# Kernel optimization log

Hardware: AMD Instinct MI355X
Metric: run time of the kernel (lower is better)

Reference implementation:

```python
import jax, jax.numpy as jnp
import numpy as np

N = 4096      # num_nodes (also node feature dim)
E = 32768     # num_edges
EMB = 8       # embedding_dim


def setup_inputs() -> dict:
    key = jax.random.key(0)
    ks = jax.random.split(key, 12)
    s = lambda fan_in: 1.0 / np.sqrt(fan_in)
    return {
        "x": jax.random.normal(ks[0], (N, N), dtype=jnp.float32),
        "edge_index": jax.random.randint(ks[1], (2, E), 0, N, dtype=jnp.int64),
        "edge_weight": jax.random.uniform(ks[2], (E,), dtype=jnp.float32),
        # GCNConv linear (PyG Linear, weight [out,in]) + bias
        "gcn_w": jax.random.normal(ks[3], (N, N), dtype=jnp.float32) * s(N),
        "gcn_b": jnp.zeros((N,), dtype=jnp.float32),
        # Wq: Linear(N -> E)
        "wq_w": jax.random.normal(ks[4], (E, N), dtype=jnp.float32) * s(N),
        "wq_b": jax.random.normal(ks[5], (E,), dtype=jnp.float32) * s(N),
        # edge embedding table [E, EMB]
        "emb": jax.random.normal(ks[6], (E, EMB), dtype=jnp.float32),
        # WF: Linear(N+EMB -> 1)
        "wf_w": jax.random.normal(ks[7], (1, N + EMB), dtype=jnp.float32) * s(N + EMB),
        "wf_b": jax.random.normal(ks[8], (1,), dtype=jnp.float32) * s(N + EMB),
    }


def reference(x, edge_index, edge_weight, gcn_w, gcn_b, wq_w, wq_b, emb, wf_w, wf_b):
    n = x.shape[0]
    row, col = edge_index[0], edge_index[1]
    # --- GCNConv: add self loops (weight 1.0), symmetric normalization ---
    loop = jnp.arange(n)
    row_f = jnp.concatenate([row, loop])
    col_f = jnp.concatenate([col, loop])
    w_f = jnp.concatenate([edge_weight, jnp.ones((n,), dtype=x.dtype)])
    deg = jax.ops.segment_sum(w_f, col_f, num_segments=n)          # weighted in-degree
    dis = jnp.where(deg > 0, jax.lax.rsqrt(deg), 0.0)              # deg^{-1/2}, 0 for isolated
    norm = dis[row_f] * w_f * dis[col_f]                           # [E+N]
    h = x @ gcn_w.T                                                # linear transform first (as PyG)
    agg = jax.ops.segment_sum(norm[:, None] * h[row_f], col_f, num_segments=n)
    H1 = jnp.tanh(agg + gcn_b)                                     # [N, N]
    # --- dense head ---
    H2 = jnp.tanh(H1 @ wq_w.T + wq_b)                              # [N, E]
    H2_t = H2.T                                                    # [E, N]
    feat = jnp.concatenate([H2_t, emb], axis=1)                    # [E, N+EMB]
    F_hat = (feat @ wf_w.T + wf_b)[:, 0]                           # [E]
    return F_hat
```

## Files before the change

kernel.cpp:

```cpp
#include <hip/hip_runtime.h>
#include <hip/hip_bf16.h>

#define NN 4096
#define NE 32768
#define NEMB 8

typedef __bf16 bf16x8 __attribute__((ext_vector_type(8)));
typedef float  f32x4  __attribute__((ext_vector_type(4)));

__device__ __forceinline__ unsigned short f2bf(float f) {
  union { float f; unsigned int u; } v; v.f = f;
  return (unsigned short)((v.u + 0x7FFFu + ((v.u >> 16) & 1u)) >> 16);
}

__global__ void k_f2bf(const float* __restrict__ in, unsigned short* __restrict__ out, long n8) {
  long i = (long)blockIdx.x * blockDim.x + threadIdx.x;
  long stride = (long)gridDim.x * blockDim.x;
  for (long j = i; j < n8; j += stride) {
    const float* p = in + j * 8;
    float4 a = *(const float4*)p;
    float4 b = *(const float4*)(p + 4);
    union { unsigned short u[8]; uint4 v; } o;
    o.u[0] = f2bf(a.x); o.u[1] = f2bf(a.y); o.u[2] = f2bf(a.z); o.u[3] = f2bf(a.w);
    o.u[4] = f2bf(b.x); o.u[5] = f2bf(b.y); o.u[6] = f2bf(b.z); o.u[7] = f2bf(b.w);
    *(uint4*)(out + j * 8) = o.v;
  }
}

__global__ void k_deg_init(float* deg) { deg[blockIdx.x * 256 + threadIdx.x] = 1.0f; }

__global__ void k_edge_accum(const int* __restrict__ ei, const float* __restrict__ ew,
                             float* deg, int* cnt) {
  int e = blockIdx.x * 256 + threadIdx.x;
  if (e >= NE) return;
  int c = ei[NE + e];
  atomicAdd(&deg[c], ew[e]);
  atomicAdd(&cnt[c], 1);
}

__global__ void k_dis(const float* __restrict__ deg, float* __restrict__ dis) {
  int i = blockIdx.x * 256 + threadIdx.x;
  float d = deg[i];
  dis[i] = d > 0.f ? rsqrtf(d) : 0.f;
}

__global__ void k_scan(const int* __restrict__ cnt, int* __restrict__ starts) {
  __shared__ int sh[1024];
  int tid = threadIdx.x;
  int base = tid * 4;
  int v[4]; int sum = 0;
  for (int i = 0; i < 4; i++) { v[i] = cnt[base + i]; sum += v[i]; }
  sh[tid] = sum;
  __syncthreads();
  for (int offd = 1; offd < 1024; offd <<= 1) {
    int t = (tid >= offd) ? sh[tid - offd] : 0;
    __syncthreads();
    sh[tid] += t;
    __syncthreads();
  }
  int run = sh[tid] - sum;
  for (int i = 0; i < 4; i++) { starts[base + i] = run; run += v[i]; }
}

__global__ void k_fill(const int* __restrict__ ei, const int* __restrict__ starts,
                       int* cursor, int* csr_e) {
  int e = blockIdx.x * 256 + threadIdx.x;
  if (e >= NE) return;
  int c = ei[NE + e];
  int pos = atomicAdd(&cursor[c], 1);
  csr_e[starts[c] + pos] = e;
}

__global__ void k_sortnorm(const int* __restrict__ ei, const float* __restrict__ ew,
                           const int* __restrict__ starts, const int* __restrict__ cnt,
                           const float* __restrict__ dis,
                           int* csr_e, int* __restrict__ csr_row, float* __restrict__ csr_nrm) {
  int n = blockIdx.x * 256 + threadIdx.x;
  if (n >= NN) return;
  int s = starts[n], c = cnt[n];
  for (int i = 1; i < c; i++) {
    int key = csr_e[s + i]; int j = i - 1;
    while (j >= 0 && csr_e[s + j] > key) { csr_e[s + j + 1] = csr_e[s + j]; j--; }
    csr_e[s + j + 1] = key;
  }
  float dn = dis[n];
  for (int i = 0; i < c; i++) {
    int e = csr_e[s + i];
    int r = ei[e];
    csr_row[s + i] = r;
    csr_nrm[s + i] = dis[r] * ew[e] * dn;
  }
}

__global__ __launch_bounds__(256) void k_agg(
    const float* __restrict__ h, const float* __restrict__ dis,
    const int* __restrict__ starts, const int* __restrict__ cnt,
    const int* __restrict__ csr_row, const float* __restrict__ csr_nrm,
    const float* __restrict__ gcn_b, unsigned short* __restrict__ H1b) {
  int n = blockIdx.x;
  int tid = threadIdx.x;
  float dn = dis[n];
  float sw = dn * dn;
  float acc[16];
  const float* hn = h + (size_t)n * NN;
  #pragma unroll
  for (int i = 0; i < 16; i++) { int f = tid + i * 256; acc[i] = sw * hn[f] + gcn_b[f]; }
  int s = starts[n], c = cnt[n];
  __shared__ int   s_row[64];
  __shared__ float s_nrm[64];
  for (int base = 0; base < c; base += 64) {
    int m = min(64, c - base);
    __syncthreads();
    if (tid < m) { s_row[tid] = csr_row[s + base + tid]; s_nrm[tid] = csr_nrm[s + base + tid]; }
    __syncthreads();
    for (int j = 0; j < m; j++) {
      const float* hr = h + (size_t)s_row[j] * NN;
      float wgt = s_nrm[j];
      #pragma unroll
      for (int i = 0; i < 16; i++) acc[i] += wgt * hr[tid + i * 256];
    }
  }
  #pragma unroll
  for (int i = 0; i < 16; i++)
    H1b[(size_t)n * NN + tid + i * 256] = f2bf(tanhf(acc[i]));
}

__device__ __forceinline__ void gload16(const void* g, void* l) {
  __builtin_amdgcn_global_load_lds(
      (const __attribute__((address_space(1))) unsigned int*)g,
      (__attribute__((address_space(3))) unsigned int*)l, 16, 0, 0);
}

#define BARX() do { __builtin_amdgcn_sched_barrier(0); __builtin_amdgcn_s_barrier(); __builtin_amdgcn_sched_barrier(0); } while (0)
#define LGKM0() do { asm volatile("s_waitcnt lgkmcnt(0)" ::: "memory"); __builtin_amdgcn_sched_barrier(0); } while (0)
#define VMC(n) do { asm volatile("s_waitcnt vmcnt(" #n ")" ::: "memory"); } while (0)


#define STAGE(buf, mat, kk, tk) do { \
    size_t off_ = (size_t)(tk) * 64 + (kk) * 32; \
    gload16((mat ? gB0 : gA0) + off_, &LDS[buf][mat][kk][c0][0]); \
    gload16((mat ? gB1 : gA1) + off_, &LDS[buf][mat][kk][c0 + 1][0]); \
  } while (0)

#define LDA4(dst, buf, kk, q) do { \
    const unsigned short* b_ = &LDS[buf][0][kk][wr * 8 + (q) * 4][0] + aoff; \
    dst[0] = *(const bf16x8*)(b_); \
    dst[1] = *(const bf16x8*)(b_ + 512); \
    dst[2] = *(const bf16x8*)(b_ + 1024); \
    dst[3] = *(const bf16x8*)(b_ + 1536); \
  } while (0)

#define LDB4(dst, buf, kk) do { \
    const unsigned short* b_ = &LDS[buf][1][kk][wc * 4][0] + aoff; \
    dst[0] = *(const bf16x8*)(b_); \
    dst[1] = *(const bf16x8*)(b_ + 512); \
    dst[2] = *(const bf16x8*)(b_ + 1024); \
    dst[3] = *(const bf16x8*)(b_ + 1536); \
  } while (0)

#define MMA16(q, av, bv) do { \
    __builtin_amdgcn_s_setprio(1); \
    _Pragma("unroll") \
    for (int mf_ = 0; mf_ < 4; mf_++) \
      _Pragma("unroll") \
      for (int nf_ = 0; nf_ < 4; nf_++) \
        acc[(q) * 4 + mf_][nf_] = __builtin_amdgcn_mfma_f32_16x16x32_bf16(av[mf_], bv[nf_], acc[(q) * 4 + mf_][nf_], 0, 0, 0); \
    __builtin_amdgcn_s_setprio(0); \
  } while (0)


template<bool FUSED>
__global__ __launch_bounds__(512, 2) void gemm8(
    const unsigned short* __restrict__ A,
    const unsigned short* __restrict__ B,
    int N, int K, int nRb,
    float* __restrict__ outF,
    const float* __restrict__ colBias,
    const float* __restrict__ rowW,
    float* __restrict__ P) {
  __shared__ unsigned short LDS[2][2][2][16][512];

  const int nwg = gridDim.x, n8 = nwg >> 3;
  const int bid = blockIdx.x;
  const int swz = (bid & 7) * n8 + (bid >> 3);
  const int rb = swz % nRb, cb = swz / nRb;
  const int row0 = rb * 256, col0 = cb * 256;

  const int tid = threadIdx.x;
  const int w = tid >> 6, l = tid & 63;
  const int wr = w >> 2, wc = w & 3;
  const int l15 = l & 15, kl = l >> 4;

  const int c0 = w * 2;
  const int pq = l >> 2;
  const int pc = (l & 3) ^ ((l >> 3) & 3);
  const unsigned short* gA0 = A + (size_t)(row0 + c0 * 16 + pq) * K + pc * 8;
  const unsigned short* gA1 = gA0 + (size_t)16 * K;
  const unsigned short* gB0 = B + (size_t)(col0 + c0 * 16 + pq) * K + pc * 8;
  const unsigned short* gB1 = gB0 + (size_t)16 * K;

  const int aoff = l15 * 32 + ((kl ^ ((l >> 1) & 3)) << 3);

  f32x4 acc[8][4];
  #pragma unroll
  for (int m = 0; m < 8; m++)
    #pragma unroll
    for (int n = 0; n < 4; n++)
      acc[m][n] = f32x4{0.f, 0.f, 0.f, 0.f};

  STAGE(0, 0, 0, 0); STAGE(0, 1, 0, 0); STAGE(0, 0, 1, 0); STAGE(0, 1, 1, 0);
  STAGE(1, 0, 0, 1); STAGE(1, 1, 0, 1);
  VMC(4);
  BARX();

  const int NIT = K >> 7;
  for (int i = 0; i < NIT; i++) {
    const int ta = 2 * i, tb = 2 * i + 1;
    const bool mid = (i < NIT - 1);
    bf16x8 av[4], bv[4];
    LDB4(bv, 0, 0); LDA4(av, 0, 0, 0);
    STAGE(1, 0, 1, tb);
    BARX(); LGKM0(); MMA16(0, av, bv); BARX();
    LDA4(av, 0, 0, 1);
    STAGE(1, 1, 1, tb);
    BARX(); LGKM0(); MMA16(1, av, bv); VMC(8); BARX();
    LDB4(bv, 0, 1); LDA4(av, 0, 1, 0);
    if (mid) STAGE(0, 0, 0, ta + 2);
    BARX(); LGKM0(); MMA16(0, av, bv); BARX();
    LDA4(av, 0, 1, 1);
    if (mid) STAGE(0, 1, 0, ta + 2);
    BARX(); LGKM0(); MMA16(1, av, bv);
    if (mid) VMC(8); else VMC(0);
    BARX();
    LDB4(bv, 1, 0); LDA4(av, 1, 0, 0);
    if (mid) STAGE(0, 0, 1, ta + 2);
    BARX(); LGKM0(); MMA16(0, av, bv); BARX();
    LDA4(av, 1, 0, 1);
    if (mid) STAGE(0, 1, 1, ta + 2);
    BARX(); LGKM0(); MMA16(1, av, bv);
    if (mid) VMC(8);
    BARX();
    LDB4(bv, 1, 1); LDA4(av, 1, 1, 0);
    if (mid) STAGE(1, 0, 0, tb + 2);
    BARX(); LGKM0(); MMA16(0, av, bv); BARX();
    LDA4(av, 1, 1, 1);
    if (mid) STAGE(1, 1, 0, tb + 2);
    BARX(); LGKM0(); MMA16(1, av, bv);
    if (mid) VMC(8);
    BARX();
  }

  if (!FUSED) {
    #pragma unroll
    for (int mf = 0; mf < 8; mf++)
      #pragma unroll
      for (int nf = 0; nf < 4; nf++) {
        int row = row0 + wr * 128 + mf * 16 + kl * 4;
        int col = col0 + wc * 64 + nf * 16 + l15;
        float* o = outF + (size_t)row * N + col;
        #pragma unroll
        for (int r = 0; r < 4; r++) o[(size_t)r * N] = acc[mf][nf][r];
      }
  } else {
    #pragma unroll
    for (int nf = 0; nf < 4; nf++) {
      int col = col0 + wc * 64 + nf * 16 + l15;
      float bias = colBias[col];
      float s = 0.f;
      #pragma unroll
      for (int mf = 0; mf < 8; mf++) {
        int rbase = row0 + wr * 128 + mf * 16 + kl * 4;
        #pragma unroll
        for (int r = 0; r < 4; r++)
          s += rowW[rbase + r] * tanhf(acc[mf][nf][r] + bias);
      }
      s += __shfl_xor(s, 16, 64);
      s += __shfl_xor(s, 32, 64);
      if (l < 16) P[(size_t)(rb * 2 + wr) * N + col] = s;
    }
  }
}

__global__ void k_final(const float* __restrict__ P, const float* __restrict__ emb,
                        const float* __restrict__ wf, const float* __restrict__ wfb,
                        float* __restrict__ out) {
  int e = blockIdx.x * 256 + threadIdx.x;
  float s = 0.f;
  for (int r = 0; r < 32; r++) s += P[(size_t)r * NE + e];
  float c = wfb[0];
  #pragma unroll
  for (int k = 0; k < NEMB; k++) c += emb[e * NEMB + k] * wf[NN + k];
  out[e] = s + c;
}

extern "C" void kernel_launch(void* const* d_in, const int* in_sizes, int n_in,
                              void* d_out, int out_size, void* d_ws, size_t ws_size,
                              hipStream_t stream) {
  const float* x    = (const float*)d_in[0];
  const int*   ei   = (const int*)d_in[1];
  const float* ew   = (const float*)d_in[2];
  const float* gcnw = (const float*)d_in[3];
  const float* gcnb = (const float*)d_in[4];
  const float* wqw  = (const float*)d_in[5];
  const float* wqb  = (const float*)d_in[6];
  const float* emb  = (const float*)d_in[7];
  const float* wfw  = (const float*)d_in[8];
  const float* wfb  = (const float*)d_in[9];
  float* out = (float*)d_out;

  char* ws = (char*)d_ws;
  size_t off = 0;
  auto alloc = [&](size_t b) { char* p = ws + off; off += (b + 255) & ~(size_t)255; return p; };

  unsigned short* wq16  = (unsigned short*)alloc((size_t)NE * NN * 2);
  float*          h     = (float*)alloc((size_t)NN * NN * 4);
  unsigned short* x16   = (unsigned short*)alloc((size_t)NN * NN * 2);
  unsigned short* w16   = (unsigned short*)alloc((size_t)NN * NN * 2);
  unsigned short* h1b   = (unsigned short*)alloc((size_t)NN * NN * 2);
  float* deg    = (float*)alloc(NN * 4);
  float* dis    = (float*)alloc(NN * 4);
  int*   cnt    = (int*)alloc(NN * 4);
  int*   cursor = (int*)alloc(NN * 4);
  int*   starts = (int*)alloc(NN * 4);
  int*   csr_e  = (int*)alloc(NE * 4);
  int*   csr_row= (int*)alloc(NE * 4);
  float* csr_nrm= (float*)alloc(NE * 4);
  float* P      = (float*)alloc((size_t)32 * NE * 4);

  hipMemsetAsync(cnt, 0, NN * 4 * 2, stream);

  k_deg_init<<<NN / 256, 256, 0, stream>>>(deg);
  k_edge_accum<<<NE / 256, 256, 0, stream>>>(ei, ew, deg, cnt);
  k_dis<<<NN / 256, 256, 0, stream>>>(deg, dis);
  k_scan<<<1, 1024, 0, stream>>>(cnt, starts);
  k_fill<<<NE / 256, 256, 0, stream>>>(ei, starts, cursor, csr_e);
  k_sortnorm<<<NN / 256, 256, 0, stream>>>(ei, ew, starts, cnt, dis, csr_e, csr_row, csr_nrm);

  k_f2bf<<<1024, 256, 0, stream>>>(x, x16, (long)NN * NN / 8);
  k_f2bf<<<1024, 256, 0, stream>>>(gcnw, w16, (long)NN * NN / 8);
  k_f2bf<<<2048, 256, 0, stream>>>(wqw, wq16, (long)NE * NN / 8);

  gemm8<false><<<16 * 16, 512, 0, stream>>>(x16, w16, NN, NN, 16, h, nullptr, nullptr, nullptr);

  k_agg<<<NN, 256, 0, stream>>>(h, dis, starts, cnt, csr_row, csr_nrm, gcnb, h1b);

  gemm8<true><<<16 * 128, 512, 0, stream>>>(h1b, wq16, NE, NN, 16, nullptr, wqb, wfw, P);

  k_final<<<NE / 256, 256, 0, stream>>>(P, emb, wfw, wfb, out);
}
```

Before: 1.450 ms.

## Double-buffer LDS fragment registers to overlap ds_reads with MFMA

Splits the A/B fragment registers into two sets so the next fragment's LDS reads are issued before the current MFMA block. Waits use partial lgkmcnt counts instead of draining to zero, and the vmcnt waits are retimed to match. The first fragments are prefetched before the loop, and the last iteration is peeled into a separate branch. This hides LDS read latency behind matrix math, at the cost of more VGPRs and more fragile wait-count bookkeeping under the 512-thread, 2-blocks-per-CU launch bounds.

```diff
diff --git a/kernel.cpp b/kernel.cpp
--- a/kernel.cpp
+++ b/kernel.cpp
@@ -132,7 +132,7 @@
 }
 
 #define BARX() do { __builtin_amdgcn_sched_barrier(0); __builtin_amdgcn_s_barrier(); __builtin_amdgcn_sched_barrier(0); } while (0)
-#define LGKM0() do { asm volatile("s_waitcnt lgkmcnt(0)" ::: "memory"); __builtin_amdgcn_sched_barrier(0); } while (0)
+#define LGKM(n) do { asm volatile("s_waitcnt lgkmcnt(" #n ")" ::: "memory"); __builtin_amdgcn_sched_barrier(0); } while (0)
 #define VMC(n) do { asm volatile("s_waitcnt vmcnt(" #n ")" ::: "memory"); } while (0)
 
 
@@ -167,7 +167,6 @@
         acc[(q) * 4 + mf_][nf_] = __builtin_amdgcn_mfma_f32_16x16x32_bf16(av[mf_], bv[nf_], acc[(q) * 4 + mf_][nf_], 0, 0, 0); \
     __builtin_amdgcn_s_setprio(0); \
   } while (0)
-
 
 template<bool FUSED>
 __global__ __launch_bounds__(512, 2) void gemm8(
@@ -208,46 +207,50 @@
     for (int n = 0; n < 4; n++)
       acc[m][n] = f32x4{0.f, 0.f, 0.f, 0.f};
 
+  bf16x8 avA[4], avB[4], bvA[4], bvB[4];
+
   STAGE(0, 0, 0, 0); STAGE(0, 1, 0, 0); STAGE(0, 0, 1, 0); STAGE(0, 1, 1, 0);
   STAGE(1, 0, 0, 1); STAGE(1, 1, 0, 1);
   VMC(4);
   BARX();
+  LDB4(bvA, 0, 0); LDA4(avA, 0, 0, 0);
 
   const int NIT = K >> 7;
   for (int i = 0; i < NIT; i++) {
     const int ta = 2 * i, tb = 2 * i + 1;
     const bool mid = (i < NIT - 1);
-    bf16x8 av[4], bv[4];
-    LDB4(bv, 0, 0); LDA4(av, 0, 0, 0);
+    LDA4(avB, 0, 0, 1);
     STAGE(1, 0, 1, tb);
-    BARX(); LGKM0(); MMA16(0, av, bv); BARX();
-    LDA4(av, 0, 0, 1);
+    BARX(); LGKM(4); MMA16(0, avA, bvA); VMC(6); BARX();
+    LDB4(bvB, 0, 1); LDA4(avA, 0, 1, 0);
     STAGE(1, 1, 1, tb);
-    BARX(); LGKM0(); MMA16(1, av, bv); VMC(8); BARX();
-    LDB4(bv, 0, 1); LDA4(av, 0, 1, 0);
+    BARX(); LGKM(8); MMA16(1, avB, bvA); BARX();
+    LDA4(avB, 0, 1, 1);
     if (mid) STAGE(0, 0, 0, ta + 2);
-    BARX(); LGKM0(); MMA16(0, av, bv); BARX();
-    LDA4(av, 0, 1, 1);
+    BARX(); LGKM(4); MMA16(0, avA, bvB);
+    if (mid) VMC(6); else VMC(4);
+    BARX();
+    LDB4(bvA, 1, 0); LDA4(avA, 1, 0, 0);
     if (mid) STAGE(0, 1, 0, ta + 2);
-    BARX(); LGKM0(); MMA16(1, av, bv);
-    if (mid) VMC(8); else VMC(0);
+    BARX(); LGKM(8); MMA16(1, avB, bvB); BARX();
+    LDA4(avB, 1, 0, 1);
+    if (mid) STAGE(0, 0, 1, ta + 2);
+    BARX(); LGKM(4); MMA16(0, avA, bvA);
+    if (mid) VMC(6); else VMC(0);
     BARX();
-    LDB4(bv, 1, 0); LDA4(av, 1, 0, 0);
-    if (mid) STAGE(0, 0, 1, ta + 2);
-    BARX(); LGKM0(); MMA16(0, av, bv); BARX();
-    LDA4(av, 1, 0, 1);
+    LDB4(bvB, 1, 1); LDA4(avA, 1, 1, 0);
     if (mid) STAGE(0, 1, 1, ta + 2);
-    BARX(); LGKM0(); MMA16(1, av, bv);
-    if (mid) VMC(8);
-    BARX();
-    LDB4(bv, 1, 1); LDA4(av, 1, 1, 0);
+    BARX(); LGKM(8); MMA16(1, avB, bvA); BARX();
+    LDA4(avB, 1, 1, 1);
     if (mid) STAGE(1, 0, 0, tb + 2);
-    BARX(); LGKM0(); MMA16(0, av, bv); BARX();
-    LDA4(av, 1, 1, 1);
-    if (mid) STAGE(1, 1, 0, tb + 2);
-    BARX(); LGKM0(); MMA16(1, av, bv);
-    if (mid) VMC(8);
-    BARX();
+    BARX(); LGKM(4); MMA16(0, avA, bvB); VMC(6); BARX();
+    if (mid) {
+      LDB4(bvA, 0, 0); LDA4(avA, 0, 0, 0);
+      STAGE(1, 1, 0, tb + 2);
+      BARX(); LGKM(8); MMA16(1, avB, bvB); BARX();
+    } else {
+      BARX(); LGKM(0); MMA16(1, avB, bvB); BARX();
+    }
   }
 
   if (!FUSED) {
```

Measured after the change: 3.121 ms. 2.15x slower.
